# Optimization experiments

Measured on AMD Instinct MI355X. Metric: run time of the kernel, lower is better.

Reference implementation:

```python
import jax, jax.numpy as jnp
import numpy as np


def setup_inputs() -> dict:
    key = jax.random.key(0)
    kx, ky = jax.random.split(key)
    B, n, d = 2, 2048, 64
    x = jax.random.normal(kx, (B, n, d), dtype=jnp.float32)
    y = jax.random.normal(ky, (B, n, d), dtype=jnp.float32)
    return {"x": x, "y": y}


def reference(x, y):
    # Pairwise squared Euclidean distance: out[b,i,j] = sum_d (x[b,i,d]-y[b,j,d])^2
    # Same math as torch broadcast+cat+pow+sum, expressed via broadcasting.
    diff = x[:, :, None, :] - y[:, None, :, :]  # [B, n, n, d]
    return jnp.sum(diff * diff, axis=-1)  # [B, n, n]
```

## Files before the change

kernel.cpp:

```cpp
#include <hip/hip_runtime.h>
#include <hip/hip_bf16.h>

typedef __attribute__((ext_vector_type(8))) short bf16x8;
typedef __attribute__((ext_vector_type(4))) float f32x4;
typedef __attribute__((ext_vector_type(4))) short s16x4;

#define LDSS 72

__device__ __forceinline__ short f2bf(float f) {
    union { float f; unsigned u; } v; v.f = f;
    unsigned r = v.u + 0x7fffu + ((v.u >> 16) & 1u);
    return (short)(r >> 16);
}

__global__ __launch_bounds__(256) void pdist_kernel(
    const float* __restrict__ x, const float* __restrict__ y,
    float* __restrict__ out, int n)
{
    constexpr int D = 64;
    __shared__ short xs[128 * LDSS];
    __shared__ short ys[128 * LDSS];
    __shared__ float xn[128];
    __shared__ float yn[128];

    const int b  = blockIdx.z;
    const int i0 = blockIdx.y * 128;
    const int j0 = blockIdx.x * 128;
    const float* xb = x + ((size_t)b * n + i0) * D;
    const float* yb = y + ((size_t)b * n + j0) * D;

    const int t = threadIdx.x;

    const f32x4* xv = (const f32x4*)xb;
    const f32x4* yv = (const f32x4*)yb;
    #pragma unroll
    for (int c = 0; c < 8; ++c) {
        int idx  = t + c * 256;
        int row  = idx >> 4;
        int col4 = (idx & 15) << 2;
        f32x4 vx = xv[idx];
        f32x4 vy = yv[idx];
        s16x4 sx = { f2bf(vx.x), f2bf(vx.y), f2bf(vx.z), f2bf(vx.w) };
        s16x4 sy = { f2bf(vy.x), f2bf(vy.y), f2bf(vy.z), f2bf(vy.w) };
        *(s16x4*)&xs[row * LDSS + col4] = sx;
        *(s16x4*)&ys[row * LDSS + col4] = sy;
    }

    {
        int r = t & 127;
        const f32x4* p = (const f32x4*)((t < 128 ? xb : yb) + r * D);
        float s = 0.f;
        #pragma unroll
        for (int c = 0; c < 16; ++c) {
            f32x4 v = p[c];
            s += v.x * v.x + v.y * v.y + v.z * v.z + v.w * v.w;
        }
        if (t < 128) xn[r] = s; else yn[r] = s;
    }

    __syncthreads();

    const int lane = t & 63;
    const int w    = t >> 6;
    const int wi   = (w >> 1) * 64;
    const int wj   = (w & 1)  * 64;
    const int lrow = lane & 15;
    const int quad = lane >> 4;

    const short* xbase = &xs[(wi + lrow) * LDSS + quad * 8];
    const short* ybase = &ys[(wj + lrow) * LDSS + quad * 8];

    bf16x8 af[4][2], bf[4][2];
    #pragma unroll
    for (int ti = 0; ti < 4; ++ti) {
        af[ti][0] = *(const bf16x8*)(xbase + ti * 16 * LDSS);
        af[ti][1] = *(const bf16x8*)(xbase + ti * 16 * LDSS + 32);
        bf[ti][0] = *(const bf16x8*)(ybase + ti * 16 * LDSS);
        bf[ti][1] = *(const bf16x8*)(ybase + ti * 16 * LDSS + 32);
    }

    f32x4 acc[4][4];
    #pragma unroll
    for (int ti = 0; ti < 4; ++ti)
        #pragma unroll
        for (int tj = 0; tj < 4; ++tj) {
            f32x4 z = {0.f, 0.f, 0.f, 0.f};
            z = __builtin_amdgcn_mfma_f32_16x16x32_bf16(af[ti][0], bf[tj][0], z, 0, 0, 0);
            z = __builtin_amdgcn_mfma_f32_16x16x32_bf16(af[ti][1], bf[tj][1], z, 0, 0, 0);
            acc[ti][tj] = z;
        }

    float* outb = out + (size_t)b * n * n;
    #pragma unroll
    for (int ti = 0; ti < 4; ++ti) {
        #pragma unroll
        for (int tj = 0; tj < 4; ++tj) {
            int gj   = j0 + wj + tj * 16 + lrow;
            float yv_ = yn[wj + tj * 16 + lrow];
            #pragma unroll
            for (int r = 0; r < 4; ++r) {
                int li = wi + ti * 16 + quad * 4 + r;
                int gi = i0 + li;
                float v = xn[li] + yv_ - 2.0f * acc[ti][tj][r];
                outb[(size_t)gi * n + gj] = v;
            }
        }
    }
}

extern "C" void kernel_launch(void* const* d_in, const int* in_sizes, int n_in,
                              void* d_out, int out_size, void* d_ws, size_t ws_size,
                              hipStream_t stream) {
    const float* x = (const float*)d_in[0];
    const float* y = (const float*)d_in[1];
    float* out = (float*)d_out;

    const long long n = ((long long)out_size * 64) / in_sizes[0];
    const long long B = (long long)in_sizes[0] / (n * 64);

    dim3 grid((unsigned)(n / 128), (unsigned)(n / 128), (unsigned)B);
    pdist_kernel<<<grid, 256, 0, stream>>>(x, y, out, (int)n);
}
```

Before: 72.65 us.

## Retile to 64x256 blocks and stage epilogue through LDS for coalesced float4 stores

```diff
diff --git a/kernel.cpp b/kernel.cpp
--- a/kernel.cpp
+++ b/kernel.cpp
@@ -6,6 +6,7 @@
 typedef __attribute__((ext_vector_type(4))) short s16x4;
 
 #define LDSS 72
+#define EST  260
 
 __device__ __forceinline__ short f2bf(float f) {
     union { float f; unsigned u; } v; v.f = f;
@@ -17,66 +18,61 @@
     const float* __restrict__ x, const float* __restrict__ y,
     float* __restrict__ out, int n)
 {
-    constexpr int D = 64;
-    __shared__ short xs[128 * LDSS];
-    __shared__ short ys[128 * LDSS];
-    __shared__ float xn[128];
-    __shared__ float yn[128];
+    __shared__ union {
+        short stage[(64 + 256) * LDSS];
+        float ep[32 * EST];
+    } u;
+    __shared__ float xn[64];
+    __shared__ float yn[256];
 
     const int b  = blockIdx.z;
-    const int i0 = blockIdx.y * 128;
-    const int j0 = blockIdx.x * 128;
-    const float* xb = x + ((size_t)b * n + i0) * D;
-    const float* yb = y + ((size_t)b * n + j0) * D;
-
+    const int i0 = blockIdx.y * 64;
+    const int j0 = blockIdx.x * 256;
+    const float* xb = x + ((size_t)b * n + i0) * 64;
+    const float* yb = y + ((size_t)b * n + j0) * 64;
     const int t = threadIdx.x;
 
-    const f32x4* xv = (const f32x4*)xb;
-    const f32x4* yv = (const f32x4*)yb;
-    #pragma unroll
-    for (int c = 0; c < 8; ++c) {
-        int idx  = t + c * 256;
-        int row  = idx >> 4;
-        int col4 = (idx & 15) << 2;
-        f32x4 vx = xv[idx];
-        f32x4 vy = yv[idx];
-        s16x4 sx = { f2bf(vx.x), f2bf(vx.y), f2bf(vx.z), f2bf(vx.w) };
-        s16x4 sy = { f2bf(vy.x), f2bf(vy.y), f2bf(vy.z), f2bf(vy.w) };
-        *(s16x4*)&xs[row * LDSS + col4] = sx;
-        *(s16x4*)&ys[row * LDSS + col4] = sy;
-    }
-
     {
-        int r = t & 127;
-        const f32x4* p = (const f32x4*)((t < 128 ? xb : yb) + r * D);
+        const f32x4* p = (const f32x4*)yb + (size_t)t * 16;
         float s = 0.f;
         #pragma unroll
         for (int c = 0; c < 16; ++c) {
             f32x4 v = p[c];
             s += v.x * v.x + v.y * v.y + v.z * v.z + v.w * v.w;
+            s16x4 sv = { f2bf(v.x), f2bf(v.y), f2bf(v.z), f2bf(v.w) };
+            *(s16x4*)&u.stage[(64 + t) * LDSS + c * 4] = sv;
         }
-        if (t < 128) xn[r] = s; else yn[r] = s;
+        yn[t] = s;
     }
-
+    if (t < 64) {
+        const f32x4* p = (const f32x4*)xb + (size_t)t * 16;
+        float s = 0.f;
+        #pragma unroll
+        for (int c = 0; c < 16; ++c) {
+            f32x4 v = p[c];
+            s += v.x * v.x + v.y * v.y + v.z * v.z + v.w * v.w;
+            s16x4 sv = { f2bf(v.x), f2bf(v.y), f2bf(v.z), f2bf(v.w) };
+            *(s16x4*)&u.stage[t * LDSS + c * 4] = sv;
+        }
+        xn[t] = s;
+    }
     __syncthreads();
 
     const int lane = t & 63;
     const int w    = t >> 6;
-    const int wi   = (w >> 1) * 64;
-    const int wj   = (w & 1)  * 64;
     const int lrow = lane & 15;
     const int quad = lane >> 4;
 
-    const short* xbase = &xs[(wi + lrow) * LDSS + quad * 8];
-    const short* ybase = &ys[(wj + lrow) * LDSS + quad * 8];
+    const short* xbase = &u.stage[lrow * LDSS + quad * 8];
+    const short* ybase = &u.stage[(64 + w * 64 + lrow) * LDSS + quad * 8];
 
-    bf16x8 af[4][2], bf[4][2];
+    bf16x8 ax[4][2], by[4][2];
     #pragma unroll
     for (int ti = 0; ti < 4; ++ti) {
-        af[ti][0] = *(const bf16x8*)(xbase + ti * 16 * LDSS);
-        af[ti][1] = *(const bf16x8*)(xbase + ti * 16 * LDSS + 32);
-        bf[ti][0] = *(const bf16x8*)(ybase + ti * 16 * LDSS);
-        bf[ti][1] = *(const bf16x8*)(ybase + ti * 16 * LDSS + 32);
+        ax[ti][0] = *(const bf16x8*)(xbase + ti * 16 * LDSS);
+        ax[ti][1] = *(const bf16x8*)(xbase + ti * 16 * LDSS + 32);
+        by[ti][0] = *(const bf16x8*)(ybase + ti * 16 * LDSS);
+        by[ti][1] = *(const bf16x8*)(ybase + ti * 16 * LDSS + 32);
     }
 
     f32x4 acc[4][4];
@@ -85,25 +81,39 @@
         #pragma unroll
         for (int tj = 0; tj < 4; ++tj) {
             f32x4 z = {0.f, 0.f, 0.f, 0.f};
-            z = __builtin_amdgcn_mfma_f32_16x16x32_bf16(af[ti][0], bf[tj][0], z, 0, 0, 0);
-            z = __builtin_amdgcn_mfma_f32_16x16x32_bf16(af[ti][1], bf[tj][1], z, 0, 0, 0);
+            z = __builtin_amdgcn_mfma_f32_16x16x32_bf16(by[tj][0], ax[ti][0], z, 0, 0, 0);
+            z = __builtin_amdgcn_mfma_f32_16x16x32_bf16(by[tj][1], ax[ti][1], z, 0, 0, 0);
             acc[ti][tj] = z;
         }
 
     float* outb = out + (size_t)b * n * n;
     #pragma unroll
-    for (int ti = 0; ti < 4; ++ti) {
+    for (int c = 0; c < 2; ++c) {
+        __syncthreads();
         #pragma unroll
-        for (int tj = 0; tj < 4; ++tj) {
-            int gj   = j0 + wj + tj * 16 + lrow;
-            float yv_ = yn[wj + tj * 16 + lrow];
+        for (int tt = 0; tt < 2; ++tt) {
+            const int ti = c * 2 + tt;
+            const float xv = xn[ti * 16 + lrow];
             #pragma unroll
-            for (int r = 0; r < 4; ++r) {
-                int li = wi + ti * 16 + quad * 4 + r;
-                int gi = i0 + li;
-                float v = xn[li] + yv_ - 2.0f * acc[ti][tj][r];
-                outb[(size_t)gi * n + gj] = v;
+            for (int tj = 0; tj < 4; ++tj) {
+                const int jb = w * 64 + tj * 16 + quad * 4;
+                f32x4 yv = *(const f32x4*)&yn[jb];
+                f32x4 a  = acc[ti][tj];
+                f32x4 v  = { xv + yv.x - 2.0f * a.x,
+                             xv + yv.y - 2.0f * a.y,
+                             xv + yv.z - 2.0f * a.z,
+                             xv + yv.w - 2.0f * a.w };
+                *(f32x4*)&u.ep[(tt * 16 + lrow) * EST + jb] = v;
             }
+        }
+        __syncthreads();
+        #pragma unroll
+        for (int it = 0; it < 8; ++it) {
+            const int idx  = t + it * 256;
+            const int row  = idx >> 6;
+            const int col4 = (idx & 63) << 2;
+            f32x4 v = *(const f32x4*)&u.ep[row * EST + col4];
+            *(f32x4*)&outb[(size_t)(i0 + c * 32 + row) * n + (j0 + col4)] = v;
         }
     }
 }
@@ -118,6 +128,6 @@
     const long long n = ((long long)out_size * 64) / in_sizes[0];
     const long long B = (long long)in_sizes[0] / (n * 64);
 
-    dim3 grid((unsigned)(n / 128), (unsigned)(n / 128), (unsigned)B);
+    dim3 grid((unsigned)(n / 256), (unsigned)(n / 64), (unsigned)B);
     pdist_kernel<<<grid, 256, 0, stream>>>(x, y, out, (int)n);
 }
```

Measured after the change: 75.04 us. +3.3%, slower.

## Load MFMA operands directly from global, swap operands for vectorized output stores

Applied to the files above, without the earlier changes.

```diff
diff --git a/kernel.cpp b/kernel.cpp
--- a/kernel.cpp
+++ b/kernel.cpp
@@ -3,9 +3,6 @@
 
 typedef __attribute__((ext_vector_type(8))) short bf16x8;
 typedef __attribute__((ext_vector_type(4))) float f32x4;
-typedef __attribute__((ext_vector_type(4))) short s16x4;
-
-#define LDSS 72
 
 __device__ __forceinline__ short f2bf(float f) {
     union { float f; unsigned u; } v; v.f = f;
@@ -17,66 +14,60 @@
     const float* __restrict__ x, const float* __restrict__ y,
     float* __restrict__ out, int n)
 {
-    constexpr int D = 64;
-    __shared__ short xs[128 * LDSS];
-    __shared__ short ys[128 * LDSS];
-    __shared__ float xn[128];
-    __shared__ float yn[128];
-
-    const int b  = blockIdx.z;
-    const int i0 = blockIdx.y * 128;
-    const int j0 = blockIdx.x * 128;
-    const float* xb = x + ((size_t)b * n + i0) * D;
-    const float* yb = y + ((size_t)b * n + j0) * D;
-
-    const int t = threadIdx.x;
-
-    const f32x4* xv = (const f32x4*)xb;
-    const f32x4* yv = (const f32x4*)yb;
-    #pragma unroll
-    for (int c = 0; c < 8; ++c) {
-        int idx  = t + c * 256;
-        int row  = idx >> 4;
-        int col4 = (idx & 15) << 2;
-        f32x4 vx = xv[idx];
-        f32x4 vy = yv[idx];
-        s16x4 sx = { f2bf(vx.x), f2bf(vx.y), f2bf(vx.z), f2bf(vx.w) };
-        s16x4 sy = { f2bf(vy.x), f2bf(vy.y), f2bf(vy.z), f2bf(vy.w) };
-        *(s16x4*)&xs[row * LDSS + col4] = sx;
-        *(s16x4*)&ys[row * LDSS + col4] = sy;
-    }
-
-    {
-        int r = t & 127;
-        const f32x4* p = (const f32x4*)((t < 128 ? xb : yb) + r * D);
-        float s = 0.f;
-        #pragma unroll
-        for (int c = 0; c < 16; ++c) {
-            f32x4 v = p[c];
-            s += v.x * v.x + v.y * v.y + v.z * v.z + v.w * v.w;
-        }
-        if (t < 128) xn[r] = s; else yn[r] = s;
-    }
-
-    __syncthreads();
-
+    const int b    = blockIdx.z;
+    const int i0   = blockIdx.y * 64;
+    const int j0   = blockIdx.x * 256;
+    const int t    = threadIdx.x;
     const int lane = t & 63;
     const int w    = t >> 6;
-    const int wi   = (w >> 1) * 64;
-    const int wj   = (w & 1)  * 64;
     const int lrow = lane & 15;
     const int quad = lane >> 4;
 
-    const short* xbase = &xs[(wi + lrow) * LDSS + quad * 8];
-    const short* ybase = &ys[(wj + lrow) * LDSS + quad * 8];
+    const float* xb = x + ((size_t)b * n + i0) * 64;
+    const float* yb = y + ((size_t)b * n + j0 + w * 64) * 64;
 
-    bf16x8 af[4][2], bf[4][2];
+    bf16x8 ax[4][2]; float xnrm[4];
     #pragma unroll
     for (int ti = 0; ti < 4; ++ti) {
-        af[ti][0] = *(const bf16x8*)(xbase + ti * 16 * LDSS);
-        af[ti][1] = *(const bf16x8*)(xbase + ti * 16 * LDSS + 32);
-        bf[ti][0] = *(const bf16x8*)(ybase + ti * 16 * LDSS);
-        bf[ti][1] = *(const bf16x8*)(ybase + ti * 16 * LDSS + 32);
+        const float* p = xb + (size_t)(ti * 16 + lrow) * 64 + quad * 8;
+        f32x4 v0 = *(const f32x4*)p;
+        f32x4 v1 = *(const f32x4*)(p + 4);
+        f32x4 v2 = *(const f32x4*)(p + 32);
+        f32x4 v3 = *(const f32x4*)(p + 36);
+        float s = v0.x*v0.x + v0.y*v0.y + v0.z*v0.z + v0.w*v0.w
+                + v1.x*v1.x + v1.y*v1.y + v1.z*v1.z + v1.w*v1.w
+                + v2.x*v2.x + v2.y*v2.y + v2.z*v2.z + v2.w*v2.w
+                + v3.x*v3.x + v3.y*v3.y + v3.z*v3.z + v3.w*v3.w;
+        s += __shfl_xor(s, 16);
+        s += __shfl_xor(s, 32);
+        xnrm[ti] = s;
+        bf16x8 f0 = { f2bf(v0.x), f2bf(v0.y), f2bf(v0.z), f2bf(v0.w),
+                      f2bf(v1.x), f2bf(v1.y), f2bf(v1.z), f2bf(v1.w) };
+        bf16x8 f1 = { f2bf(v2.x), f2bf(v2.y), f2bf(v2.z), f2bf(v2.w),
+                      f2bf(v3.x), f2bf(v3.y), f2bf(v3.z), f2bf(v3.w) };
+        ax[ti][0] = f0; ax[ti][1] = f1;
+    }
+
+    bf16x8 by[4][2]; float ynrm[4];
+    #pragma unroll
+    for (int tj = 0; tj < 4; ++tj) {
+        const float* p = yb + (size_t)(tj * 16 + lrow) * 64 + quad * 8;
+        f32x4 v0 = *(const f32x4*)p;
+        f32x4 v1 = *(const f32x4*)(p + 4);
+        f32x4 v2 = *(const f32x4*)(p + 32);
+        f32x4 v3 = *(const f32x4*)(p + 36);
+        float s = v0.x*v0.x + v0.y*v0.y + v0.z*v0.z + v0.w*v0.w
+                + v1.x*v1.x + v1.y*v1.y + v1.z*v1.z + v1.w*v1.w
+                + v2.x*v2.x + v2.y*v2.y + v2.z*v2.z + v2.w*v2.w
+                + v3.x*v3.x + v3.y*v3.y + v3.z*v3.z + v3.w*v3.w;
+        s += __shfl_xor(s, 16);
+        s += __shfl_xor(s, 32);
+        ynrm[tj] = s;
+        bf16x8 f0 = { f2bf(v0.x), f2bf(v0.y), f2bf(v0.z), f2bf(v0.w),
+                      f2bf(v1.x), f2bf(v1.y), f2bf(v1.z), f2bf(v1.w) };
+        bf16x8 f1 = { f2bf(v2.x), f2bf(v2.y), f2bf(v2.z), f2bf(v2.w),
+                      f2bf(v3.x), f2bf(v3.y), f2bf(v3.z), f2bf(v3.w) };
+        by[tj][0] = f0; by[tj][1] = f1;
     }
 
     f32x4 acc[4][4];
@@ -85,25 +76,29 @@
         #pragma unroll
         for (int tj = 0; tj < 4; ++tj) {
             f32x4 z = {0.f, 0.f, 0.f, 0.f};
-            z = __builtin_amdgcn_mfma_f32_16x16x32_bf16(af[ti][0], bf[tj][0], z, 0, 0, 0);
-            z = __builtin_amdgcn_mfma_f32_16x16x32_bf16(af[ti][1], bf[tj][1], z, 0, 0, 0);
+            z = __builtin_amdgcn_mfma_f32_16x16x32_bf16(by[tj][0], ax[ti][0], z, 0, 0, 0);
+            z = __builtin_amdgcn_mfma_f32_16x16x32_bf16(by[tj][1], ax[ti][1], z, 0, 0, 0);
             acc[ti][tj] = z;
         }
 
     float* outb = out + (size_t)b * n * n;
     #pragma unroll
-    for (int ti = 0; ti < 4; ++ti) {
+    for (int tj = 0; tj < 4; ++tj) {
+        f32x4 yv;
+        yv.x = __shfl(ynrm[tj], quad * 4 + 0);
+        yv.y = __shfl(ynrm[tj], quad * 4 + 1);
+        yv.z = __shfl(ynrm[tj], quad * 4 + 2);
+        yv.w = __shfl(ynrm[tj], quad * 4 + 3);
+        const int gj = j0 + w * 64 + tj * 16 + quad * 4;
         #pragma unroll
-        for (int tj = 0; tj < 4; ++tj) {
-            int gj   = j0 + wj + tj * 16 + lrow;
-            float yv_ = yn[wj + tj * 16 + lrow];
-            #pragma unroll
-            for (int r = 0; r < 4; ++r) {
-                int li = wi + ti * 16 + quad * 4 + r;
-                int gi = i0 + li;
-                float v = xn[li] + yv_ - 2.0f * acc[ti][tj][r];
-                outb[(size_t)gi * n + gj] = v;
-            }
+        for (int ti = 0; ti < 4; ++ti) {
+            const int gi = i0 + ti * 16 + lrow;
+            f32x4 a = acc[ti][tj];
+            f32x4 v = { xnrm[ti] + yv.x - 2.0f * a.x,
+                        xnrm[ti] + yv.y - 2.0f * a.y,
+                        xnrm[ti] + yv.z - 2.0f * a.z,
+                        xnrm[ti] + yv.w - 2.0f * a.w };
+            *(f32x4*)&outb[(size_t)gi * n + gj] = v;
         }
     }
 }
@@ -118,6 +113,6 @@
     const long long n = ((long long)out_size * 64) / in_sizes[0];
     const long long B = (long long)in_sizes[0] / (n * 64);
 
-    dim3 grid((unsigned)(n / 128), (unsigned)(n / 128), (unsigned)B);
+    dim3 grid((unsigned)(n / 256), (unsigned)(n / 64), (unsigned)B);
     pdist_kernel<<<grid, 256, 0, stream>>>(x, y, out, (int)n);
 }
```

New measurement: 74.75 us. 1.03x slower.
